# Kernel tuning notes

Hardware: AMD Instinct MI355X
Metric: run time of the kernel (lower is better)

## Reference

```python
import jax, jax.numpy as jnp
import numpy as np
import math

D_IN = 1024
D_OUT = 1024
NUM_HEADS = 16
HEAD_DIM = D_OUT // NUM_HEADS
B = 2
S = 4096


def setup_inputs() -> dict:
    key = jax.random.key(0)
    ks = jax.random.split(key, 6)
    x = jax.random.normal(ks[0], (B, S, D_IN), dtype=jnp.float32)
    # kaiming-uniform-ish scale for weights; exact init values don't matter for correctness
    bound = 1.0 / math.sqrt(D_IN)
    Wq = jax.random.uniform(ks[1], (D_OUT, D_IN), minval=-bound, maxval=bound, dtype=jnp.float32)
    Wk = jax.random.uniform(ks[2], (D_OUT, D_IN), minval=-bound, maxval=bound, dtype=jnp.float32)
    Wv = jax.random.uniform(ks[3], (D_OUT, D_IN), minval=-bound, maxval=bound, dtype=jnp.float32)
    Wo = jax.random.uniform(ks[4], (D_OUT, D_OUT), minval=-bound, maxval=bound, dtype=jnp.float32)
    bo = jax.random.uniform(ks[5], (D_OUT,), minval=-bound, maxval=bound, dtype=jnp.float32)
    return {"x": x, "Wq": Wq, "Wk": Wk, "Wv": Wv, "Wo": Wo, "bo": bo}


@jax.custom_vjp
def binarize(w):
    return jnp.sign(w)

def _bin_fwd(w):
    return jnp.sign(w), w

def _bin_bwd(w, g):
    # straight-through estimator: pass grad where |w| <= 1
    return (g * (jnp.abs(w) <= 1).astype(g.dtype),)

binarize.defvjp(_bin_fwd, _bin_bwd)


def reference(x, Wq, Wk, Wv, Wo, bo):
    b, n, _ = x.shape
    h, hd = NUM_HEADS, HEAD_DIM
    # binarized projections (torch F.linear: x @ W.T)
    q = (x @ binarize(Wq).T).reshape(b, n, h, hd).transpose(0, 2, 1, 3)  # [b,h,n,hd]
    k = (x @ binarize(Wk).T).reshape(b, n, h, hd).transpose(0, 2, 1, 3)
    v = (x @ binarize(Wv).T).reshape(b, n, h, hd).transpose(0, 2, 1, 3)
    scores = jnp.einsum('bhqd,bhkd->bhqk', q, k) / math.sqrt(hd)  # [b,h,n,n]
    causal = jnp.tril(jnp.ones((n, n), dtype=bool))
    scores = jnp.where(causal, scores, -jnp.inf)
    attn = jax.nn.softmax(scores, axis=-1)
    # dropout p=0.0 -> identity
    ctx = jnp.einsum('bhqk,bhkd->bqhd', attn, v).reshape(b, n, h * hd)
    return ctx @ binarize(Wo).T + bo
```

## Files before the change

kernel.cpp:

```cpp
#include <hip/hip_runtime.h>
#include <hip/hip_bf16.h>
#include <cstdint>
#include <cstddef>

#define S 4096
#define D 1024
#define H 16
#define HD 64
#define BATCH 2
#define M_TOK 8192
#define K2 2048

typedef short short8 __attribute__((ext_vector_type(8)));
typedef __bf16 bf16x8 __attribute__((ext_vector_type(8)));
typedef float f32x4 __attribute__((ext_vector_type(4)));
typedef unsigned int u32;

static __device__ __forceinline__ ushort f2bf(float f) {
  union { float f; uint32_t u; } v; v.f = f;
  uint32_t u = v.u + 0x7FFFu + ((v.u >> 16) & 1u);
  return (ushort)(u >> 16);
}
static __device__ __forceinline__ float bf2f(ushort h) {
  union { uint32_t u; float f; } v; v.u = ((uint32_t)h) << 16; return v.f;
}
static __device__ __forceinline__ uint32_t cvtpk(float lo, float hi) {
  uint32_t r;
  asm("v_cvt_pk_bf16_f32 %0, %1, %2" : "=v"(r) : "v"(lo), "v"(hi));
  return r;
}
static __device__ __forceinline__ float vexp2(float x) {
  float r;
  asm("v_exp_f32 %0, %1" : "=v"(r) : "v"(x));
  return r;
}
static __device__ __forceinline__ bf16x8 pack4(uint32_t a, uint32_t b, uint32_t c, uint32_t d) {
  union { uint32_t u[4]; bf16x8 v; } z;
  z.u[0] = a; z.u[1] = b; z.u[2] = c; z.u[3] = d;
  return z.v;
}
static __device__ __forceinline__ void gld16(const void* g, void* l) {
  __builtin_amdgcn_global_load_lds(
      (const __attribute__((address_space(1))) u32*)g,
      (__attribute__((address_space(3))) u32*)l, 16, 0, 0);
}
static __device__ __forceinline__ ushort sgn(float a) {
  return a > 0.f ? 0x3F80 : (a < 0.f ? 0xBF80 : 0);
}

__global__ void prep_x(const float* __restrict__ x, ushort* __restrict__ xcat) {
  int i = blockIdx.x * blockDim.x + threadIdx.x;
  const int total = M_TOK * 128;
  for (; i < total; i += gridDim.x * blockDim.x) {
    int row = i >> 7, c8 = (i & 127) * 8;
    const float* px = &x[(size_t)row * 1024 + c8];
    float4 a = *(const float4*)px;
    float4 b = *(const float4*)(px + 4);
    float va[8] = {a.x, a.y, a.z, a.w, b.x, b.y, b.z, b.w};
    union { ushort u[8]; short8 v; } Hh, Ll;
#pragma unroll
    for (int j = 0; j < 8; ++j) {
      ushort h = f2bf(va[j]);
      Hh.u[j] = h;
      Ll.u[j] = f2bf(va[j] - bf2f(h));
    }
    *(short8*)&xcat[(size_t)row * K2 + c8] = Hh.v;
    *(short8*)&xcat[(size_t)row * K2 + 1024 + c8] = Ll.v;
  }
}

__global__ void prep_w(const float* __restrict__ wq, const float* __restrict__ wk,
                       const float* __restrict__ wv, const float* __restrict__ wo,
                       ushort* __restrict__ wcat, ushort* __restrict__ wob) {
  int i = blockIdx.x * blockDim.x + threadIdx.x;
  const int total = (D * D) / 4;
  for (; i < total; i += gridDim.x * blockDim.x) {
    float4 a;
    union { ushort u[4]; uint2 v; } t;
    a = *(const float4*)&wq[i * 4];
    t.u[0] = sgn(a.x); t.u[1] = sgn(a.y); t.u[2] = sgn(a.z); t.u[3] = sgn(a.w);
    *(uint2*)&wcat[i * 4] = t.v;
    a = *(const float4*)&wk[i * 4];
    t.u[0] = sgn(a.x); t.u[1] = sgn(a.y); t.u[2] = sgn(a.z); t.u[3] = sgn(a.w);
    *(uint2*)&wcat[D * D + i * 4] = t.v;
    a = *(const float4*)&wv[i * 4];
    t.u[0] = sgn(a.x); t.u[1] = sgn(a.y); t.u[2] = sgn(a.z); t.u[3] = sgn(a.w);
    *(uint2*)&wcat[2 * D * D + i * 4] = t.v;
    a = *(const float4*)&wo[i * 4];
    t.u[0] = sgn(a.x); t.u[1] = sgn(a.y); t.u[2] = sgn(a.z); t.u[3] = sgn(a.w);
    *(uint2*)&wob[i * 4] = t.v;
  }
}

__global__ __launch_bounds__(512, 2) void gemm256(
    const ushort* __restrict__ A, const ushort* __restrict__ Bw,
    ushort* __restrict__ q_hi, ushort* __restrict__ q_lo,
    ushort* __restrict__ k_hi, ushort* __restrict__ k_lo)
{
  __shared__ ushort smA[3][256 * 32];
  __shared__ ushort smB[3][256 * 32];
  const int tid = threadIdx.x;
  const int l = tid & 63;
  const int w = tid >> 6;
  const int x = l & 15, g = l >> 4;
  const int wm = w >> 2, wn = w & 3;
  const int bm = blockIdx.x, bn = blockIdx.y;

  const ushort* gA[2]; const ushort* gB[2]; int ldso[2];
#pragma unroll
  for (int r = 0; r < 2; ++r) {
    int q = r * 512 + tid;
    int row = q >> 2;
    int blk = (q & 3) ^ ((row & 3) ^ ((row >> 2) & 3));
    gA[r] = &A[(size_t)(bm * 256 + row) * 2048 + blk * 8];
    gB[r] = &Bw[(size_t)(bn * 256 + row) * 1024 + blk * 8];
    ldso[r] = (r * 512 + w * 64) * 8;
  }

  f32x4 acc[8][4] = {};

#pragma unroll
  for (int r = 0; r < 2; ++r) {
    gld16(gA[r] + 0, &smA[0][ldso[r]]);
    gld16(gB[r] + 0, &smB[0][ldso[r]]);
  }
#pragma unroll
  for (int r = 0; r < 2; ++r) {
    gld16(gA[r] + 32, &smA[1][ldso[r]]);
    gld16(gB[r] + ((32) & 1023), &smB[1][ldso[r]]);
  }

  const int swz = (x & 3) ^ ((x >> 2) & 3);
  int cb = 0;
  for (int s = 0; s < 64; ++s) {
    if (s < 63) {
      asm volatile("s_waitcnt vmcnt(4)" ::: "memory");
    } else {
      asm volatile("s_waitcnt vmcnt(0)" ::: "memory");
    }
    __builtin_amdgcn_s_barrier();

    if (s + 2 < 64) {
      int nb = cb - 1; if (nb < 0) nb = 2;
      int k0 = (s + 2) * 32;
#pragma unroll
      for (int r = 0; r < 2; ++r) {
        gld16(gA[r] + k0, &smA[nb][ldso[r]]);
        gld16(gB[r] + (k0 & 1023), &smB[nb][ldso[r]]);
      }
    }

    const ushort* bA = smA[cb];
    const ushort* bB = smB[cb];
    bf16x8 af[8], bf_[4];
#pragma unroll
    for (int m = 0; m < 8; ++m)
      af[m] = *(const bf16x8*)&bA[(wm * 128 + m * 16 + x) * 32 + (g ^ swz) * 8];
#pragma unroll
    for (int n = 0; n < 4; ++n)
      bf_[n] = *(const bf16x8*)&bB[(wn * 64 + n * 16 + x) * 32 + (g ^ swz) * 8];

    __builtin_amdgcn_s_setprio(1);
#pragma unroll
    for (int m = 0; m < 8; ++m)
#pragma unroll
      for (int n = 0; n < 4; ++n)
        acc[m][n] = __builtin_amdgcn_mfma_f32_16x16x32_bf16(af[m], bf_[n], acc[m][n], 0, 0, 0);
    __builtin_amdgcn_s_setprio(0);

    cb = (cb == 2) ? 0 : cb + 1;
  }

#pragma unroll
  for (int m = 0; m < 8; ++m)
#pragma unroll
    for (int n = 0; n < 4; ++n)
#pragma unroll
      for (int r = 0; r < 4; ++r) {
        int rowg = bm * 256 + wm * 128 + m * 16 + g * 4 + r;
        int colg = bn * 256 + wn * 64 + n * 16 + x;
        float v = acc[m][n][r];
        int bi = rowg >> 12, ntok = rowg & 4095;
        int proj = colg >> 10;
        int cg = colg & 1023;
        int h = cg >> 6, hd = cg & 63;
        ushort* oh = (proj == 0) ? q_hi : k_hi;
        ushort* ol = (proj == 0) ? q_lo : k_lo;
        size_t off = (size_t)(bi * H + h) * (S * HD) + (size_t)ntok * HD + hd;
        ushort hiv = f2bf(v);
        oh[off] = hiv;
        ol[off] = f2bf(v - bf2f(hiv));
      }
}

template<int EPI, int KK, int BROW, int AST>
__global__ __launch_bounds__(256) void gemm97(
    const ushort* __restrict__ A, const ushort* __restrict__ Bw,
    ushort* __restrict__ v_t,
    float* __restrict__ of, const float* __restrict__ bias)
{
  __shared__ ushort smA[128 * 32];
  __shared__ ushort smB[128 * 32];
  const int tid = threadIdx.x;
  const int l = tid & 63;
  const int w = tid >> 6;
  const int x = l & 15, g = l >> 4;
  const int wm = w >> 1, wn = w & 1;
  const int bm = blockIdx.x, bn = blockIdx.y;

  const ushort* gA[2]; const ushort* gB[2]; int ldso[2];
#pragma unroll
  for (int p = 0; p < 2; ++p) {
    int q = p * 256 + tid;
    gA[p] = &A[(size_t)(bm * 128 + (q >> 2)) * AST + (q & 3) * 8];
    gB[p] = &Bw[(size_t)(bn * 128 + (q >> 2)) * BROW + (q & 3) * 8];
    ldso[p] = (p * 256 + w * 64) * 8;
  }

  f32x4 acc[4][4] = {};

  for (int k0 = 0; k0 < KK; k0 += 32) {
    __syncthreads();
#pragma unroll
    for (int p = 0; p < 2; ++p) {
      gld16(gA[p] + k0, &smA[ldso[p]]);
      gld16(gB[p] + (k0 & (BROW - 1)), &smB[ldso[p]]);
    }
    __syncthreads();
    bf16x8 af[4], bf_[4];
#pragma unroll
    for (int m = 0; m < 4; ++m)
      af[m] = *(const bf16x8*)&smA[(wm * 64 + m * 16 + x) * 32 + g * 8];
#pragma unroll
    for (int n = 0; n < 4; ++n)
      bf_[n] = *(const bf16x8*)&smB[(wn * 64 + n * 16 + x) * 32 + g * 8];
#pragma unroll
    for (int m = 0; m < 4; ++m)
#pragma unroll
      for (int n = 0; n < 4; ++n)
        acc[m][n] = __builtin_amdgcn_mfma_f32_16x16x32_bf16(af[m], bf_[n], acc[m][n], 0, 0, 0);
  }

#pragma unroll
  for (int m = 0; m < 4; ++m)
#pragma unroll
    for (int n = 0; n < 4; ++n)
#pragma unroll
      for (int r = 0; r < 4; ++r) {
        int rowg = bm * 128 + wm * 64 + m * 16 + g * 4 + r;
        int colg = bn * 128 + wn * 64 + n * 16 + x;
        float v = acc[m][n][r];
        if (EPI == 2) {
          of[(size_t)rowg * D + colg] = v + bias[colg];
        } else {
          int bi = rowg >> 12, ntok = rowg & 4095;
          int cg = colg & 1023;
          int h = cg >> 6, hd = cg & 63;
          size_t bhb = (size_t)(bi * H + h) * (S * HD);
          int t5 = ntok & 31;
          int pos = ((t5 >> 2) & 3) * 8 + ((t5 >> 4) & 1) * 4 + (t5 & 3);
          v_t[bhb + (size_t)hd * S + (ntok & ~31) + pos] = f2bf(v);
        }
      }
}

__global__ __launch_bounds__(256) void flash5(
    const ushort* __restrict__ qhi, const ushort* __restrict__ qlo,
    const ushort* __restrict__ khi, const ushort* __restrict__ klo,
    const ushort* __restrict__ vt, ushort* __restrict__ ctx)
{
  __shared__ ushort smKhi[2][64 * 64];
  __shared__ ushort smKlo[2][64 * 64];
  __shared__ ushort smVT[2][64 * 64];

  const int tid = threadIdx.x;
  const int l = tid & 63;
  const int w = tid >> 6;
  const int x = l & 15;
  const int g = l >> 4;
  const int bh = blockIdx.x;
  const int qt = (int)(gridDim.y - 1) - (int)blockIdx.y;
  const int qbase = qt * 128;
  const size_t qkbase = (size_t)bh * S * HD;

  int soff_k[2]; size_t soff_v[2]; int ldso[2];
#pragma unroll
  for (int p = 0; p < 2; ++p) {
    int q = p * 256 + tid;
    int r2 = q >> 3;
    int sb = (q & 7) ^ (r2 & 7);
    soff_k[p] = r2 * HD + sb * 8;
    soff_v[p] = (size_t)r2 * S + sb * 8;
    ldso[p] = (p * 256 + w * 64) * 8;
  }
  const ushort* khb = khi + qkbase;
  const ushort* klb = klo + qkbase;
  const ushort* vtb = vt + qkbase;

  bf16x8 bq[2][2][2];
#pragma unroll
  for (int qs = 0; qs < 2; ++qs) {
    int qrow = qbase + w * 32 + qs * 16 + x;
    size_t base = qkbase + (size_t)qrow * HD + g * 8;
    bq[qs][0][0] = *(const bf16x8*)&qhi[base];
    bq[qs][0][1] = *(const bf16x8*)&qhi[base + 32];
    bq[qs][1][0] = *(const bf16x8*)&qlo[base];
    bq[qs][1][1] = *(const bf16x8*)&qlo[base + 32];
  }

  float mrun[2] = {-1e30f, -1e30f};
  float lrun[2] = {0.f, 0.f};
  f32x4 oacc[2][4] = {};

  const int kvmax = (qbase + 127) >> 6;
  const int qmaxw = qbase + w * 32 + 31;
  const float C1 = 0.125f * 1.44269504f;
  const float TH = 8.0f / C1;

#pragma unroll
  for (int p = 0; p < 2; ++p) {
    gld16(khb + soff_k[p], &smKhi[0][ldso[p]]);
    gld16(klb + soff_k[p], &smKlo[0][ldso[p]]);
    gld16(vtb + soff_v[p], &smVT[0][ldso[p]]);
  }
  __syncthreads();

  int cur = 0;
  for (int kv = 0; kv <= kvmax; ++kv) {
    if (kv < kvmax) {
      const ushort* kh = khb + (size_t)(kv + 1) * (64 * HD);
      const ushort* kl = klb + (size_t)(kv + 1) * (64 * HD);
      const ushort* vp = vtb + (size_t)(kv + 1) * 64;
      int nb = cur ^ 1;
#pragma unroll
      for (int p = 0; p < 2; ++p) {
        gld16(kh + soff_k[p], &smKhi[nb][ldso[p]]);
        gld16(kl + soff_k[p], &smKlo[nb][ldso[p]]);
        gld16(vp + soff_v[p], &smVT[nb][ldso[p]]);
      }
    }

    if (kv * 64 <= qmaxw) {
      const ushort* bKhi = smKhi[cur];
      const ushort* bKlo = smKlo[cur];
      const ushort* bVT = smVT[cur];

      f32x4 scq[2][4];
      __builtin_amdgcn_s_setprio(1);
#pragma unroll
      for (int t = 0; t < 4; ++t) {
        f32x4 a0 = {}, a1 = {};
#pragma unroll
        for (int c = 0; c < 2; ++c) {
          int pb = (t * 16 + x) * 64 + ((4 * c + g) ^ (x & 7)) * 8;
          bf16x8 kH = *(const bf16x8*)&bKhi[pb];
          bf16x8 kL = *(const bf16x8*)&bKlo[pb];
          a0 = __builtin_amdgcn_mfma_f32_16x16x32_bf16(kH, bq[0][0][c], a0, 0, 0, 0);
          a0 = __builtin_amdgcn_mfma_f32_16x16x32_bf16(kL, bq[0][0][c], a0, 0, 0, 0);
          a0 = __builtin_amdgcn_mfma_f32_16x16x32_bf16(kH, bq[0][1][c], a0, 0, 0, 0);
          a1 = __builtin_amdgcn_mfma_f32_16x16x32_bf16(kH, bq[1][0][c], a1, 0, 0, 0);
          a1 = __builtin_amdgcn_mfma_f32_16x16x32_bf16(kL, bq[1][0][c], a1, 0, 0, 0);
          a1 = __builtin_amdgcn_mfma_f32_16x16x32_bf16(kH, bq[1][1][c], a1, 0, 0, 0);
        }
        scq[0][t] = a0; scq[1][t] = a1;
      }
      __builtin_amdgcn_s_setprio(0);

      const bool needmask = (kv * 64 + 63 > qbase + w * 32);
      uint32_t pbq[2][2][4];

#pragma unroll
      for (int qs = 0; qs < 2; ++qs) {
        if (needmask) {
          int qglob = qbase + w * 32 + qs * 16 + x;
          int kb = kv * 64 + 4 * g;
#pragma unroll
          for (int t = 0; t < 4; ++t)
#pragma unroll
            for (int r = 0; r < 4; ++r)
              if (kb + t * 16 + r > qglob) scq[qs][t][r] = -1e30f;
        }
        float mt[4];
#pragma unroll
        for (int t = 0; t < 4; ++t)
          mt[t] = fmaxf(fmaxf(scq[qs][t][0], scq[qs][t][1]),
                        fmaxf(scq[qs][t][2], scq[qs][t][3]));
        float mloc = fmaxf(fmaxf(mt[0], mt[1]), fmaxf(mt[2], mt[3]));
        if (__any(mloc > mrun[qs] + TH)) {
          mloc = fmaxf(mloc, __shfl_xor(mloc, 16));
          mloc = fmaxf(mloc, __shfl_xor(mloc, 32));
          float mnew = fmaxf(mrun[qs], mloc);
          float scal = vexp2((mrun[qs] - mnew) * C1);
          mrun[qs] = mnew;
          lrun[qs] *= scal;
#pragma unroll
          for (int dt = 0; dt < 4; ++dt) oacc[qs][dt] *= scal;
        }
        float mc = mrun[qs] * C1;
#pragma unroll
        for (int t = 0; t < 4; ++t)
#pragma unroll
          for (int r = 0; r < 4; ++r)
            scq[qs][t][r] = vexp2(scq[qs][t][r] * C1 - mc);
        float st[4];
#pragma unroll
        for (int t = 0; t < 4; ++t)
          st[t] = (scq[qs][t][0] + scq[qs][t][1]) + (scq[qs][t][2] + scq[qs][t][3]);
        lrun[qs] += (st[0] + st[1]) + (st[2] + st[3]);
#pragma unroll
        for (int c = 0; c < 2; ++c) {
          pbq[qs][c][0] = cvtpk(scq[qs][2 * c][0], scq[qs][2 * c][1]);
          pbq[qs][c][1] = cvtpk(scq[qs][2 * c][2], scq[qs][2 * c][3]);
          pbq[qs][c][2] = cvtpk(scq[qs][2 * c + 1][0], scq[qs][2 * c + 1][1]);
          pbq[qs][c][3] = cvtpk(scq[qs][2 * c + 1][2], scq[qs][2 * c + 1][3]);
        }
      }

      __builtin_amdgcn_s_setprio(1);
#pragma unroll
      for (int c = 0; c < 2; ++c)
#pragma unroll
        for (int dt = 0; dt < 4; ++dt) {
          bf16x8 vf = *(const bf16x8*)&bVT[(dt * 16 + x) * 64 + ((4 * c + g) ^ (x & 7)) * 8];
          oacc[0][dt] = __builtin_amdgcn_mfma_f32_16x16x32_bf16(
              vf, pack4(pbq[0][c][0], pbq[0][c][1], pbq[0][c][2], pbq[0][c][3]), oacc[0][dt], 0, 0, 0);
          oacc[1][dt] = __builtin_amdgcn_mfma_f32_16x16x32_bf16(
              vf, pack4(pbq[1][c][0], pbq[1][c][1], pbq[1][c][2], pbq[1][c][3]), oacc[1][dt], 0, 0, 0);
        }
      __builtin_amdgcn_s_setprio(0);
    }

    __syncthreads();
    cur ^= 1;
  }

  const int b = bh >> 4, h = bh & 15;
#pragma unroll
  for (int qs = 0; qs < 2; ++qs) {
    float ls = lrun[qs];
    ls += __shfl_xor(ls, 16);
    ls += __shfl_xor(ls, 32);
    float inv = 1.0f / ls;
    int tok = qbase + w * 32 + qs * 16 + x;
#pragma unroll
    for (int dt = 0; dt < 4; ++dt) {
      uint2 uu;
      uu.x = cvtpk(oacc[qs][dt][0] * inv, oacc[qs][dt][1] * inv);
      uu.y = cvtpk(oacc[qs][dt][2] * inv, oacc[qs][dt][3] * inv);
      *(uint2*)&ctx[(size_t)(b * S + tok) * D + h * 64 + dt * 16 + 4 * g] = uu;
    }
  }
}

extern "C" void kernel_launch(void* const* d_in, const int* in_sizes, int n_in,
                              void* d_out, int out_size, void* d_ws, size_t ws_size,
                              hipStream_t stream) {
  const float* x  = (const float*)d_in[0];
  const float* Wq = (const float*)d_in[1];
  const float* Wk = (const float*)d_in[2];
  const float* Wv = (const float*)d_in[3];
  const float* Wo = (const float*)d_in[4];
  const float* bo = (const float*)d_in[5];
  float* out = (float*)d_out;

  if (ws_size < (size_t)120 * 1024 * 1024) return;

  char* ws = (char*)d_ws;
  const size_t MB = 1024 * 1024;
  ushort* xcat = (ushort*)(ws);
  ushort* ctx  = (ushort*)(ws);
  ushort* wcat = (ushort*)(ws + 32 * MB);
  ushort* wob  = (ushort*)(ws + 38 * MB);
  ushort* qhi  = (ushort*)(ws + 40 * MB);
  ushort* qlo  = (ushort*)(ws + 56 * MB);
  ushort* khi  = (ushort*)(ws + 72 * MB);
  ushort* klo  = (ushort*)(ws + 88 * MB);
  ushort* vt   = (ushort*)(ws + 104 * MB);

  prep_x<<<2048, 256, 0, stream>>>(x, xcat);
  prep_w<<<1024, 256, 0, stream>>>(Wq, Wk, Wv, Wo, wcat, wob);

  gemm256<<<dim3(32, 8), 512, 0, stream>>>(xcat, wcat, qhi, qlo, khi, klo);
  gemm97<1, 1024, 1024, 2048><<<dim3(64, 8), 256, 0, stream>>>(
      xcat, wcat + 2 * D * D, vt, nullptr, nullptr);

  flash5<<<dim3(BATCH * H, S / 128), 256, 0, stream>>>(qhi, qlo, khi, klo, vt, ctx);

  gemm97<2, 1024, 1024, 1024><<<dim3(64, 8), 256, 0, stream>>>(
      ctx, wob, nullptr, out, bo);
}
```

Baseline: 324.3 us.

## Switch flash attention to 32x32x16 MFMA tiles with permlane swap

```diff
diff --git a/kernel.cpp b/kernel.cpp
--- a/kernel.cpp
+++ b/kernel.cpp
@@ -14,6 +14,7 @@
 typedef short short8 __attribute__((ext_vector_type(8)));
 typedef __bf16 bf16x8 __attribute__((ext_vector_type(8)));
 typedef float f32x4 __attribute__((ext_vector_type(4)));
+typedef float f32x16 __attribute__((ext_vector_type(16)));
 typedef unsigned int u32;
 
 static __device__ __forceinline__ ushort f2bf(float f) {
@@ -257,14 +258,12 @@
           int cg = colg & 1023;
           int h = cg >> 6, hd = cg & 63;
           size_t bhb = (size_t)(bi * H + h) * (S * HD);
-          int t5 = ntok & 31;
-          int pos = ((t5 >> 2) & 3) * 8 + ((t5 >> 4) & 1) * 4 + (t5 & 3);
-          v_t[bhb + (size_t)hd * S + (ntok & ~31) + pos] = f2bf(v);
-        }
-      }
-}
-
-__global__ __launch_bounds__(256) void flash5(
+          v_t[bhb + (size_t)hd * S + ntok] = f2bf(v);
+        }
+      }
+}
+
+__global__ __launch_bounds__(256) void flash16(
     const ushort* __restrict__ qhi, const ushort* __restrict__ qlo,
     const ushort* __restrict__ khi, const ushort* __restrict__ klo,
     const ushort* __restrict__ vt, ushort* __restrict__ ctx)
@@ -276,8 +275,9 @@
   const int tid = threadIdx.x;
   const int l = tid & 63;
   const int w = tid >> 6;
-  const int x = l & 15;
-  const int g = l >> 4;
+  const int q31 = l & 31;
+  const int g2 = l >> 5;
+  const int l7 = l & 7;
   const int bh = blockIdx.x;
   const int qt = (int)(gridDim.y - 1) - (int)blockIdx.y;
   const int qbase = qt * 128;
@@ -297,20 +297,20 @@
   const ushort* klb = klo + qkbase;
   const ushort* vtb = vt + qkbase;
 
-  bf16x8 bq[2][2][2];
-#pragma unroll
-  for (int qs = 0; qs < 2; ++qs) {
-    int qrow = qbase + w * 32 + qs * 16 + x;
-    size_t base = qkbase + (size_t)qrow * HD + g * 8;
-    bq[qs][0][0] = *(const bf16x8*)&qhi[base];
-    bq[qs][0][1] = *(const bf16x8*)&qhi[base + 32];
-    bq[qs][1][0] = *(const bf16x8*)&qlo[base];
-    bq[qs][1][1] = *(const bf16x8*)&qlo[base + 32];
-  }
-
-  float mrun[2] = {-1e30f, -1e30f};
-  float lrun[2] = {0.f, 0.f};
-  f32x4 oacc[2][4] = {};
+  bf16x8 bq[2][4];
+  {
+    int qrow = qbase + w * 32 + q31;
+    size_t base = qkbase + (size_t)qrow * HD + g2 * 8;
+#pragma unroll
+    for (int s2 = 0; s2 < 4; ++s2) {
+      bq[0][s2] = *(const bf16x8*)&qhi[base + s2 * 16];
+      bq[1][s2] = *(const bf16x8*)&qlo[base + s2 * 16];
+    }
+  }
+
+  float mrun = -1e30f;
+  float lrun = 0.f;
+  f32x16 oacc0 = {}, oacc1 = {};
 
   const int kvmax = (qbase + 127) >> 6;
   const int qmaxw = qbase + w * 32 + 31;
@@ -345,88 +345,102 @@
       const ushort* bKlo = smKlo[cur];
       const ushort* bVT = smVT[cur];
 
-      f32x4 scq[2][4];
+      f32x16 sc0 = {}, sc1 = {};
       __builtin_amdgcn_s_setprio(1);
 #pragma unroll
-      for (int t = 0; t < 4; ++t) {
-        f32x4 a0 = {}, a1 = {};
-#pragma unroll
-        for (int c = 0; c < 2; ++c) {
-          int pb = (t * 16 + x) * 64 + ((4 * c + g) ^ (x & 7)) * 8;
+      for (int s2 = 0; s2 < 4; ++s2) {
+        {
+          int row = q31;
+          int pb = row * 64 + (((2 * s2 + g2)) ^ l7) * 8;
           bf16x8 kH = *(const bf16x8*)&bKhi[pb];
           bf16x8 kL = *(const bf16x8*)&bKlo[pb];
-          a0 = __builtin_amdgcn_mfma_f32_16x16x32_bf16(kH, bq[0][0][c], a0, 0, 0, 0);
-          a0 = __builtin_amdgcn_mfma_f32_16x16x32_bf16(kL, bq[0][0][c], a0, 0, 0, 0);
-          a0 = __builtin_amdgcn_mfma_f32_16x16x32_bf16(kH, bq[0][1][c], a0, 0, 0, 0);
-          a1 = __builtin_amdgcn_mfma_f32_16x16x32_bf16(kH, bq[1][0][c], a1, 0, 0, 0);
-          a1 = __builtin_amdgcn_mfma_f32_16x16x32_bf16(kL, bq[1][0][c], a1, 0, 0, 0);
-          a1 = __builtin_amdgcn_mfma_f32_16x16x32_bf16(kH, bq[1][1][c], a1, 0, 0, 0);
-        }
-        scq[0][t] = a0; scq[1][t] = a1;
+          sc0 = __builtin_amdgcn_mfma_f32_32x32x16_bf16(kH, bq[0][s2], sc0, 0, 0, 0);
+          sc0 = __builtin_amdgcn_mfma_f32_32x32x16_bf16(kL, bq[0][s2], sc0, 0, 0, 0);
+          sc0 = __builtin_amdgcn_mfma_f32_32x32x16_bf16(kH, bq[1][s2], sc0, 0, 0, 0);
+        }
+        {
+          int row = 32 + q31;
+          int pb = row * 64 + (((2 * s2 + g2)) ^ l7) * 8;
+          bf16x8 kH = *(const bf16x8*)&bKhi[pb];
+          bf16x8 kL = *(const bf16x8*)&bKlo[pb];
+          sc1 = __builtin_amdgcn_mfma_f32_32x32x16_bf16(kH, bq[0][s2], sc1, 0, 0, 0);
+          sc1 = __builtin_amdgcn_mfma_f32_32x32x16_bf16(kL, bq[0][s2], sc1, 0, 0, 0);
+          sc1 = __builtin_amdgcn_mfma_f32_32x32x16_bf16(kH, bq[1][s2], sc1, 0, 0, 0);
+        }
       }
       __builtin_amdgcn_s_setprio(0);
 
-      const bool needmask = (kv * 64 + 63 > qbase + w * 32);
-      uint32_t pbq[2][2][4];
-
-#pragma unroll
-      for (int qs = 0; qs < 2; ++qs) {
-        if (needmask) {
-          int qglob = qbase + w * 32 + qs * 16 + x;
-          int kb = kv * 64 + 4 * g;
-#pragma unroll
-          for (int t = 0; t < 4; ++t)
-#pragma unroll
-            for (int r = 0; r < 4; ++r)
-              if (kb + t * 16 + r > qglob) scq[qs][t][r] = -1e30f;
-        }
-        float mt[4];
-#pragma unroll
-        for (int t = 0; t < 4; ++t)
-          mt[t] = fmaxf(fmaxf(scq[qs][t][0], scq[qs][t][1]),
-                        fmaxf(scq[qs][t][2], scq[qs][t][3]));
-        float mloc = fmaxf(fmaxf(mt[0], mt[1]), fmaxf(mt[2], mt[3]));
-        if (__any(mloc > mrun[qs] + TH)) {
-          mloc = fmaxf(mloc, __shfl_xor(mloc, 16));
-          mloc = fmaxf(mloc, __shfl_xor(mloc, 32));
-          float mnew = fmaxf(mrun[qs], mloc);
-          float scal = vexp2((mrun[qs] - mnew) * C1);
-          mrun[qs] = mnew;
-          lrun[qs] *= scal;
-#pragma unroll
-          for (int dt = 0; dt < 4; ++dt) oacc[qs][dt] *= scal;
-        }
-        float mc = mrun[qs] * C1;
-#pragma unroll
-        for (int t = 0; t < 4; ++t)
-#pragma unroll
-          for (int r = 0; r < 4; ++r)
-            scq[qs][t][r] = vexp2(scq[qs][t][r] * C1 - mc);
-        float st[4];
-#pragma unroll
-        for (int t = 0; t < 4; ++t)
-          st[t] = (scq[qs][t][0] + scq[qs][t][1]) + (scq[qs][t][2] + scq[qs][t][3]);
-        lrun[qs] += (st[0] + st[1]) + (st[2] + st[3]);
-#pragma unroll
-        for (int c = 0; c < 2; ++c) {
-          pbq[qs][c][0] = cvtpk(scq[qs][2 * c][0], scq[qs][2 * c][1]);
-          pbq[qs][c][1] = cvtpk(scq[qs][2 * c][2], scq[qs][2 * c][3]);
-          pbq[qs][c][2] = cvtpk(scq[qs][2 * c + 1][0], scq[qs][2 * c + 1][1]);
-          pbq[qs][c][3] = cvtpk(scq[qs][2 * c + 1][2], scq[qs][2 * c + 1][3]);
+      if (kv * 64 + 63 > qbase + w * 32) {
+        int qglob = qbase + w * 32 + q31;
+        int kb = kv * 64 + 4 * g2;
+#pragma unroll
+        for (int r = 0; r < 16; ++r) {
+          int k5 = (r & 3) + 8 * (r >> 2);
+          if (kb + k5 > qglob) sc0[r] = -1e30f;
+          if (kb + 32 + k5 > qglob) sc1[r] = -1e30f;
+        }
+      }
+
+      float mt[8];
+#pragma unroll
+      for (int r = 0; r < 8; ++r)
+        mt[r] = fmaxf(fmaxf(sc0[2 * r], sc0[2 * r + 1]), fmaxf(sc1[2 * r], sc1[2 * r + 1]));
+      float mloc = fmaxf(fmaxf(fmaxf(mt[0], mt[1]), fmaxf(mt[2], mt[3])),
+                         fmaxf(fmaxf(mt[4], mt[5]), fmaxf(mt[6], mt[7])));
+      if (__any(mloc > mrun + TH)) {
+        float mx = fmaxf(mloc, __shfl_xor(mloc, 32));
+        float mnew = fmaxf(mrun, mx);
+        float scal = vexp2((mrun - mnew) * C1);
+        mrun = mnew;
+        lrun *= scal;
+        oacc0 *= scal;
+        oacc1 *= scal;
+      }
+      float mc = mrun * C1;
+#pragma unroll
+      for (int r = 0; r < 16; ++r) {
+        sc0[r] = vexp2(sc0[r] * C1 - mc);
+        sc1[r] = vexp2(sc1[r] * C1 - mc);
+      }
+      float st[8];
+#pragma unroll
+      for (int r = 0; r < 8; ++r)
+        st[r] = (sc0[2 * r] + sc0[2 * r + 1]) + (sc1[2 * r] + sc1[2 * r + 1]);
+      lrun += ((st[0] + st[1]) + (st[2] + st[3])) + ((st[4] + st[5]) + (st[6] + st[7]));
+
+      uint32_t pbw[4][4];
+#pragma unroll
+      for (int s2 = 0; s2 < 4; ++s2) {
+        const int s1 = s2 & 1;
+#pragma unroll
+        for (int p = 0; p < 2; ++p) {
+          uint32_t a, b;
+          if (s2 < 2) {
+            a = cvtpk(sc0[2 * p + 8 * s1], sc0[2 * p + 1 + 8 * s1]);
+            b = cvtpk(sc0[2 * p + 4 + 8 * s1], sc0[2 * p + 5 + 8 * s1]);
+          } else {
+            a = cvtpk(sc1[2 * p + 8 * s1], sc1[2 * p + 1 + 8 * s1]);
+            b = cvtpk(sc1[2 * p + 4 + 8 * s1], sc1[2 * p + 5 + 8 * s1]);
+          }
+          asm volatile("v_permlane32_swap_b32 %0, %1" : "+v"(a), "+v"(b));
+          pbw[s2][p] = a;
+          pbw[s2][2 + p] = b;
         }
       }
 
       __builtin_amdgcn_s_setprio(1);
 #pragma unroll
-      for (int c = 0; c < 2; ++c)
-#pragma unroll
-        for (int dt = 0; dt < 4; ++dt) {
-          bf16x8 vf = *(const bf16x8*)&bVT[(dt * 16 + x) * 64 + ((4 * c + g) ^ (x & 7)) * 8];
-          oacc[0][dt] = __builtin_amdgcn_mfma_f32_16x16x32_bf16(
-              vf, pack4(pbq[0][c][0], pbq[0][c][1], pbq[0][c][2], pbq[0][c][3]), oacc[0][dt], 0, 0, 0);
-          oacc[1][dt] = __builtin_amdgcn_mfma_f32_16x16x32_bf16(
-              vf, pack4(pbq[1][c][0], pbq[1][c][1], pbq[1][c][2], pbq[1][c][3]), oacc[1][dt], 0, 0, 0);
-        }
+      for (int s2 = 0; s2 < 4; ++s2) {
+        bf16x8 bp = pack4(pbw[s2][0], pbw[s2][1], pbw[s2][2], pbw[s2][3]);
+        {
+          bf16x8 vf = *(const bf16x8*)&bVT[(q31)*64 + (((2 * s2 + g2)) ^ l7) * 8];
+          oacc0 = __builtin_amdgcn_mfma_f32_32x32x16_bf16(vf, bp, oacc0, 0, 0, 0);
+        }
+        {
+          bf16x8 vf = *(const bf16x8*)&bVT[(32 + q31) * 64 + (((2 * s2 + g2)) ^ l7) * 8];
+          oacc1 = __builtin_amdgcn_mfma_f32_32x32x16_bf16(vf, bp, oacc1, 0, 0, 0);
+        }
+      }
       __builtin_amdgcn_s_setprio(0);
     }
 
@@ -435,19 +449,20 @@
   }
 
   const int b = bh >> 4, h = bh & 15;
-#pragma unroll
-  for (int qs = 0; qs < 2; ++qs) {
-    float ls = lrun[qs];
-    ls += __shfl_xor(ls, 16);
-    ls += __shfl_xor(ls, 32);
+  {
+    float ls = lrun + __shfl_xor(lrun, 32);
     float inv = 1.0f / ls;
-    int tok = qbase + w * 32 + qs * 16 + x;
-#pragma unroll
-    for (int dt = 0; dt < 4; ++dt) {
+    int tok = qbase + w * 32 + q31;
+    size_t rbase = (size_t)(b * S + tok) * D + h * 64;
+#pragma unroll
+    for (int r2 = 0; r2 < 4; ++r2) {
       uint2 uu;
-      uu.x = cvtpk(oacc[qs][dt][0] * inv, oacc[qs][dt][1] * inv);
-      uu.y = cvtpk(oacc[qs][dt][2] * inv, oacc[qs][dt][3] * inv);
-      *(uint2*)&ctx[(size_t)(b * S + tok) * D + h * 64 + dt * 16 + 4 * g] = uu;
+      uu.x = cvtpk(oacc0[4 * r2] * inv, oacc0[4 * r2 + 1] * inv);
+      uu.y = cvtpk(oacc0[4 * r2 + 2] * inv, oacc0[4 * r2 + 3] * inv);
+      *(uint2*)&ctx[rbase + 8 * r2 + 4 * g2] = uu;
+      uu.x = cvtpk(oacc1[4 * r2] * inv, oacc1[4 * r2 + 1] * inv);
+      uu.y = cvtpk(oacc1[4 * r2 + 2] * inv, oacc1[4 * r2 + 3] * inv);
+      *(uint2*)&ctx[rbase + 32 + 8 * r2 + 4 * g2] = uu;
     }
   }
 }
@@ -484,7 +499,7 @@
   gemm97<1, 1024, 1024, 2048><<<dim3(64, 8), 256, 0, stream>>>(
       xcat, wcat + 2 * D * D, vt, nullptr, nullptr);
 
-  flash5<<<dim3(BATCH * H, S / 128), 256, 0, stream>>>(qhi, qlo, khi, klo, vt, ctx);
+  flash16<<<dim3(BATCH * H, S / 128), 256, 0, stream>>>(qhi, qlo, khi, klo, vt, ctx);
 
   gemm97<2, 1024, 1024, 1024><<<dim3(64, 8), 256, 0, stream>>>(
       ctx, wob, nullptr, out, bo);
```

Result: no change. 321.0 us (-1.0%).
